# Optimization experiments

Hardware: AMD Instinct MI355X
Metric: run time of the kernel (lower is better)

## Reference

```python
import jax, jax.numpy as jnp
import numpy as np

B, CIN, H, W = 256, 1280, 7, 7
A, NCLS, HID, NGT = 9, 20, 128, 40
OUT_DIM = 5 * A + NCLS  # 65


def setup_inputs() -> dict:
    key = jax.random.key(0)
    ks = jax.random.split(key, 8)
    features = jax.random.normal(ks[0], (B, CIN, H, W), jnp.float32)
    # grid: (x, y) centers of each feature cell, in feature-map coordinates
    grid = jax.random.uniform(ks[1], (B, H, W, 2), jnp.float32) * 7.0
    # GT boxes (x1, y1, x2, y2, class), padded count NGT per image
    xy1 = jax.random.uniform(ks[2], (B, NGT, 2), jnp.float32) * 5.0
    wh = jax.random.uniform(ks[3], (B, NGT, 2), jnp.float32) * 2.0 + 0.5
    cls = jax.random.randint(ks[4], (B, NGT, 1), 0, NCLS).astype(jnp.float32)
    bboxes = jnp.concatenate([xy1, xy1 + wh, cls], axis=-1)
    # anchor shapes (w, h) as in SingleStageDetector.__init__
    anc = jnp.array([[1.0, 1], [2, 2], [3, 3], [4, 4], [5, 5],
                     [2, 3], [3, 2], [3, 5], [5, 3]], jnp.float32)
    W1 = jax.random.normal(ks[5], (HID, CIN), jnp.float32) * 0.02
    b1 = jnp.zeros((HID,), jnp.float32)
    W2 = jax.random.normal(ks[6], (OUT_DIM, HID), jnp.float32) * 0.02
    b2 = jnp.zeros((OUT_DIM,), jnp.float32)
    return dict(features=features, grid=grid, bboxes=bboxes, anc=anc,
                W1=W1, b1=b1, W2=W2, b2=b2)


def reference(features, grid, bboxes, anc, W1, b1, W2, b2):
    Bx = features.shape[0]
    # --- PredictionNetwork (inference mode; dropout is identity at eval) ---
    h = jnp.einsum('bchw,oc->bohw', features, W1) + b1[None, :, None, None]
    h = jax.nn.leaky_relu(h, negative_slope=0.01)
    out = jnp.einsum('bchw,oc->bohw', h, W2) + b2[None, :, None, None]
    conf_scores = jax.nn.sigmoid(out[:, 4 * A:5 * A])          # (B, A, H, W)
    offsets = out[:, :4 * A].reshape(Bx, A, 4, H, W)
    offsets = jnp.concatenate(
        [jax.nn.sigmoid(offsets[:, :, :2]) - 0.5, offsets[:, :, 2:]], axis=2)
    class_scores = out[:, 5 * A:]                               # (B, C, H, W)
    # --- GenerateAnchor: (B, A, H, W, 4) as (x_tl, y_tl, x_br, y_br) ---
    ctr = grid[:, None]                    # (B, 1, H, W, 2)
    half = anc[None, :, None, None, :] / 2  # (1, A, 1, 1, 2)
    anchors = jnp.concatenate([ctr - half, ctr + half], axis=-1)
    # --- IoU: (B, A*H*W, N) ---
    P = anchors.reshape(Bx, -1, 4)          # (B, AHW, 4)
    gt = bboxes[..., :4]                    # (B, N, 4)
    tl = jnp.maximum(P[:, :, None, :2], gt[:, None, :, :2])
    br = jnp.minimum(P[:, :, None, 2:], gt[:, None, :, 2:])
    inter = jnp.prod(jnp.clip(br - tl, 0.0), axis=-1)  # (B, AHW, N)
    # torch code zeroes intersections for proposals with any coord <= 0
    legal = (jnp.min(P, axis=-1) > 0)[..., None]
    inter = inter * legal
    p_area = ((P[:, :, 2] - P[:, :, 0]) * (P[:, :, 3] - P[:, :, 1]))[:, :, None]
    g_area = ((gt[:, :, 2] - gt[:, :, 0]) * (gt[:, :, 3] - gt[:, :, 1]))[:, None, :]
    iou_mat = inter / (g_area + p_area - inter)
    return (conf_scores, offsets, class_scores, iou_mat)
```

## Files before the change

### kernel.cpp

```cpp
#include <hip/hip_runtime.h>


#define CIN_  1280
#define HW_   49
#define HID_  128
#define OUTD_ 65
#define NGT_  40
#define NP_   441

#define CONF_OFF 0
#define OFFS_OFF 112896
#define CLS_OFF  564480
#define IOU_OFF  815360

#define WS_W1F   0
#define WS_W2F   81920
#define WS_PART  87040
#define WS_NEED_FULL ((87040u + 3211264u) * 4u)
#define WS_NEED_MID  (81920u * 4u)

typedef __bf16 bf16x8 __attribute__((ext_vector_type(8)));
typedef float  f32x4  __attribute__((ext_vector_type(4)));

__device__ __forceinline__ unsigned pack2bf(float lo, float hi) {
    unsigned a = __float_as_uint(lo);
    unsigned b = __float_as_uint(hi);
    a = (a + 0x7FFFu + ((a >> 16) & 1u)) >> 16;
    b = (b + 0x7FFFu + ((b >> 16) & 1u)) >> 16;
    return a | (b << 16);
}
__device__ __forceinline__ float bflo(unsigned u) { return __uint_as_float(u << 16); }
__device__ __forceinline__ float bfhi(unsigned u) { return __uint_as_float(u & 0xFFFF0000u); }
__device__ __forceinline__ float sigmoidf_(float v) { return 1.f / (1.f + __expf(-v)); }

__device__ __forceinline__ bf16x8 ld_frag(const unsigned* p) {
    union { uint4 u; bf16x8 v; } x;
    x.u = *(const uint4*)p;
    return x.v;
}
__device__ __forceinline__ bf16x8 as_bf(uint4 u) {
    union { uint4 u; bf16x8 v; } x; x.u = u; return x.v;
}

__global__ __launch_bounds__(256) void prep_w1f(const float* __restrict__ W1,
                                                unsigned* __restrict__ g) {
    int X = blockIdx.x * 256 + threadIdx.x;
    int sub = X & 3, lane = (X >> 2) & 63, f = X >> 8;
    int mt = f & 7, K32 = f >> 3;
    int o = mt * 16 + (lane & 15);
    int c = K32 * 32 + (lane >> 4) * 8 + sub * 2;
    float2 v = *(const float2*)(W1 + o * CIN_ + c);
    g[X] = pack2bf(v.x, v.y);
}

__global__ __launch_bounds__(256) void prep_w2f(const float* __restrict__ W2,
                                                unsigned* __restrict__ g) {
    int X = blockIdx.x * 256 + threadIdx.x;
    int sub = X & 3, lane = (X >> 2) & 63, f = X >> 8;
    int mt2 = f % 5, ks2 = f / 5;
    int o2 = mt2 * 16 + (lane & 15);
    int c = ks2 * 32 + (lane >> 4) * 8 + sub * 2;
    unsigned val = 0;
    if (o2 < OUTD_) {
        float2 v = *(const float2*)(W2 + o2 * HID_ + c);
        val = pack2bf(v.x, v.y);
    }
    g[X] = val;
}

__global__ __launch_bounds__(256) void gemm1_partial(
    const float* __restrict__ F, const float* __restrict__ grid,
    const float* __restrict__ bbox, const float* __restrict__ anc,
    const unsigned* __restrict__ gW1f,
    unsigned* __restrict__ wsp, float* __restrict__ out)
{
    __shared__ __align__(16) unsigned smF[49 * 164];
    float* smP = (float*)smF;
    float* smG = (float*)smF + 2646;

    const int tid  = threadIdx.x;
    const int b    = blockIdx.x >> 2;
    const int ksp  = blockIdx.x & 3;
    const int lane = tid & 63;
    const int w    = tid >> 6;
    const int quad = lane >> 4;
    const int m16  = lane & 15;

    const float* Fb = F + b * (CIN_ * HW_) + ksp * 320 * HW_;

    for (int idx = tid; idx < 1960; idx += 256) {
        int cb = idx / 49;
        int hw = idx - cb * 49;
        const float* s = Fb + cb * 392 + hw;
        float v0 = s[0],   v1 = s[49],  v2 = s[98],  v3 = s[147];
        float v4 = s[196], v5 = s[245], v6 = s[294], v7 = s[343];
        uint4 pk;
        pk.x = pack2bf(v0, v1); pk.y = pack2bf(v2, v3);
        pk.z = pack2bf(v4, v5); pk.w = pack2bf(v6, v7);
        *(uint4*)(smF + hw * 164 + cb * 4) = pk;
    }
    __syncthreads();

    const int row3 = (m16 == 0) ? 48 : (m16 - 1);
    const unsigned* Bb[4] = {
        smF + m16 * 164 + quad * 4,
        smF + (16 + m16) * 164 + quad * 4,
        smF + (32 + m16) * 164 + quad * 4,
        smF + row3 * 164 + quad * 4
    };

    const int mt0 = w * 2, mt1 = mt0 + 1;
    const int K32b = ksp * 10;
    const uint4* Ap0 = (const uint4*)gW1f + (K32b * 8 + mt0) * 64 + lane;
    const uint4* Ap1 = (const uint4*)gW1f + (K32b * 8 + mt1) * 64 + lane;

    f32x4 acc0[4], acc1[4];
    #pragma unroll
    for (int nt = 0; nt < 4; ++nt) { acc0[nt] = (f32x4)(0.f); acc1[nt] = (f32x4)(0.f); }

    uint4 a0 = Ap0[0], a1 = Ap1[0];
    for (int k = 0; k < 10; ++k) {
        uint4 n0, n1;
        if (k < 9) { n0 = Ap0[(k + 1) * 512]; n1 = Ap1[(k + 1) * 512]; }
        bf16x8 A0 = as_bf(a0), A1 = as_bf(a1);
        const int co = k * 16;
        #pragma unroll
        for (int nt = 0; nt < 4; ++nt) {
            bf16x8 Bf = ld_frag(Bb[nt] + co);
            acc0[nt] = __builtin_amdgcn_mfma_f32_16x16x32_bf16(A0, Bf, acc0[nt], 0, 0, 0);
            acc1[nt] = __builtin_amdgcn_mfma_f32_16x16x32_bf16(A1, Bf, acc1[nt], 0, 0, 0);
        }
        a0 = n0; a1 = n1;
    }

    const unsigned pbase = (unsigned)(b * 4 + ksp) * 64u;
    #pragma unroll
    for (int m = 0; m < 2; ++m) {
        const f32x4* ac = m ? acc1 : acc0;
        int mtg = w * 2 + m;
        #pragma unroll
        for (int nt = 0; nt < 4; ++nt) {
            int hw = (nt < 3) ? (nt * 16 + m16) : ((m16 == 0) ? 48 : -1);
            if (hw >= 0) {
                #pragma unroll
                for (int rp = 0; rp < 2; ++rp) {
                    int op = mtg * 8 + quad * 2 + rp;
                    wsp[(pbase + op) * 49u + hw] = pack2bf(ac[nt][2 * rp], ac[nt][2 * rp + 1]);
                }
            }
        }
    }
    __syncthreads();

    for (int pp = tid; pp < NP_; pp += 256) {
        int a = pp / 49, r = pp - a * 49;
        float cx = grid[b * 98 + 2 * r], cy = grid[b * 98 + 2 * r + 1];
        float hx = anc[2 * a] * 0.5f,    hy = anc[2 * a + 1] * 0.5f;
        float x1 = cx - hx, y1 = cy - hy, x2 = cx + hx, y2 = cy + hy;
        smP[pp * 6 + 0] = x1; smP[pp * 6 + 1] = y1;
        smP[pp * 6 + 2] = x2; smP[pp * 6 + 3] = y2;
        smP[pp * 6 + 4] = (x2 - x1) * (y2 - y1);
        smP[pp * 6 + 5] = (fminf(fminf(x1, y1), fminf(x2, y2)) > 0.f) ? 1.f : 0.f;
    }
    if (tid < NGT_) {
        int g = tid;
        float x1 = bbox[b * 200 + g * 5 + 0];
        float y1 = bbox[b * 200 + g * 5 + 1];
        float x2 = bbox[b * 200 + g * 5 + 2];
        float y2 = bbox[b * 200 + g * 5 + 3];
        smG[g * 5 + 0] = x1; smG[g * 5 + 1] = y1;
        smG[g * 5 + 2] = x2; smG[g * 5 + 3] = y2;
        smG[g * 5 + 4] = (x2 - x1) * (y2 - y1);
    }
    __syncthreads();

    for (int ii = tid; ii < 4410; ii += 256) {
        int idx = ksp * 4410 + ii;
        int p = idx / 40;
        int g = idx - p * 40;
        const float* P = smP + p * 6;
        const float* G = smG + g * 5;
        float tlx = fmaxf(P[0], G[0]);
        float tly = fmaxf(P[1], G[1]);
        float brx = fminf(P[2], G[2]);
        float bry = fminf(P[3], G[3]);
        float dx = fmaxf(brx - tlx, 0.f);
        float dy = fmaxf(bry - tly, 0.f);
        float inter = dx * dy * P[5];
        out[IOU_OFF + b * (NP_ * NGT_) + idx] = inter / (G[4] + P[4] - inter);
    }
}

__global__ __launch_bounds__(320) void gemm2_epilogue(
    const unsigned* __restrict__ wsp, const unsigned* __restrict__ gW2f,
    const float* __restrict__ B1, const float* __restrict__ B2,
    float* __restrict__ out)
{
    __shared__ __align__(16) unsigned smHT[49 * 68];

    const int tid  = threadIdx.x;
    const int b    = blockIdx.x;
    const int lane = tid & 63;
    const int w    = tid >> 6;
    const int quad = lane >> 4;
    const int m16  = lane & 15;

    const uint4* Aw2 = (const uint4*)gW2f + w * 64 + lane;
    uint4 af0 = Aw2[0], af1 = Aw2[320], af2 = Aw2[640], af3 = Aw2[960];

    const unsigned* pb = wsp + b * 12544;
    for (int j = tid; j < 3136; j += 320) {
        int op = j / 49;
        int hw = j - op * 49;
        const unsigned* p = pb + op * 49 + hw;
        unsigned u0 = p[0], u1 = p[3136], u2 = p[6272], u3 = p[9408];
        float v0 = ((bflo(u0) + bflo(u1)) + (bflo(u2) + bflo(u3))) + B1[2 * op];
        float v1 = ((bfhi(u0) + bfhi(u1)) + (bfhi(u2) + bfhi(u3))) + B1[2 * op + 1];
        v0 = v0 > 0.f ? v0 : 0.01f * v0;
        v1 = v1 > 0.f ? v1 : 0.01f * v1;
        smHT[hw * 68 + op] = pack2bf(v0, v1);
    }
    __syncthreads();

    const int row3 = (m16 == 0) ? 48 : (m16 - 1);
    const unsigned* Bb[4] = {
        smHT + m16 * 68 + quad * 4,
        smHT + (16 + m16) * 68 + quad * 4,
        smHT + (32 + m16) * 68 + quad * 4,
        smHT + row3 * 68 + quad * 4
    };
    f32x4 acc[4];
    #pragma unroll
    for (int nt = 0; nt < 4; ++nt) acc[nt] = (f32x4)(0.f);
    uint4 afs[4] = { af0, af1, af2, af3 };
    #pragma unroll
    for (int ks2 = 0; ks2 < 4; ++ks2) {
        bf16x8 A = as_bf(afs[ks2]);
        const int co = ks2 * 16;
        #pragma unroll
        for (int nt = 0; nt < 4; ++nt) {
            bf16x8 Bf = ld_frag(Bb[nt] + co);
            acc[nt] = __builtin_amdgcn_mfma_f32_16x16x32_bf16(A, Bf, acc[nt], 0, 0, 0);
        }
    }

    #pragma unroll
    for (int nt = 0; nt < 4; ++nt) {
        int hw = (nt < 3) ? (nt * 16 + m16) : ((m16 == 0) ? 48 : -1);
        if (hw < 0) continue;
        #pragma unroll
        for (int r = 0; r < 4; ++r) {
            int o2 = w * 16 + quad * 4 + r;
            if (o2 >= OUTD_) continue;
            float a = acc[nt][r] + B2[o2];
            unsigned dst; float val;
            if (o2 < 36) {
                int an = o2 >> 2, kk = o2 & 3;
                val = (kk < 2) ? (sigmoidf_(a) - 0.5f) : a;
                dst = OFFS_OFF + b * 1764 + an * 196 + kk * 49 + hw;
            } else if (o2 < 45) {
                val = sigmoidf_(a);
                dst = CONF_OFF + b * 441 + (o2 - 36) * 49 + hw;
            } else {
                val = a;
                dst = CLS_OFF + b * 980 + (o2 - 45) * 49 + hw;
            }
            out[dst] = val;
        }
    }
}

#define SF_STRIDE 644
__global__ __launch_bounds__(512) void fused_single(
    const float* __restrict__ F, const float* __restrict__ grid,
    const float* __restrict__ bbox, const float* __restrict__ anc,
    const unsigned* __restrict__ gW1f, const float* __restrict__ B1,
    const float* __restrict__ W2, const float* __restrict__ B2,
    float* __restrict__ out)
{
    __shared__ __align__(16) unsigned lds[49 * SF_STRIDE];
    unsigned* smF = lds;
    unsigned* smH = lds;
    float* smP = (float*)(lds + 3136);
    float* smG = (float*)(lds + 3136 + 2646);

    const int tid  = threadIdx.x;
    const int b    = blockIdx.x;
    const int lane = tid & 63;
    const int w    = tid >> 6;
    const int quad = lane >> 4;
    const int m16  = lane & 15;
    const float* Fb = F + b * (CIN_ * HW_);

    for (int i = tid; i < 640 * 49; i += 512) {
        int cp = i / 49;
        int hw = i - cp * 49;
        const float* s = Fb + (2 * cp) * HW_ + hw;
        smF[hw * SF_STRIDE + cp] = pack2bf(s[0], s[HW_]);
    }
    __syncthreads();

    const int row3 = (m16 == 0) ? 48 : (m16 - 1);
    const unsigned* Bb[4] = {
        smF + m16 * SF_STRIDE + quad * 4,
        smF + (16 + m16) * SF_STRIDE + quad * 4,
        smF + (32 + m16) * SF_STRIDE + quad * 4,
        smF + row3 * SF_STRIDE + quad * 4
    };
    const uint4* Aw = (const uint4*)gW1f + w * 64 + lane;

    f32x4 acc[4];
    #pragma unroll
    for (int nt = 0; nt < 4; ++nt) acc[nt] = (f32x4)(0.f);

    uint4 a0 = Aw[0], a1 = Aw[512];
    for (int ch = 0; ch < 20; ++ch) {
        uint4 n0, n1;
        if (ch < 19) { n0 = Aw[(ch + 1) * 1024]; n1 = Aw[(ch + 1) * 1024 + 512]; }
        const int coff = ch * 32;
        bf16x8 A0 = as_bf(a0), A1 = as_bf(a1);
        #pragma unroll
        for (int nt = 0; nt < 4; ++nt) {
            bf16x8 b0 = ld_frag(Bb[nt] + coff);
            bf16x8 b1 = ld_frag(Bb[nt] + coff + 16);
            acc[nt] = __builtin_amdgcn_mfma_f32_16x16x32_bf16(A0, b0, acc[nt], 0, 0, 0);
            acc[nt] = __builtin_amdgcn_mfma_f32_16x16x32_bf16(A1, b1, acc[nt], 0, 0, 0);
        }
        a0 = n0; a1 = n1;
    }
    __syncthreads();

    #pragma unroll
    for (int nt = 0; nt < 4; ++nt) {
        int hw = (nt < 3) ? (nt * 16 + m16) : ((m16 == 0) ? 48 : -1);
        if (hw >= 0) {
            #pragma unroll
            for (int rp = 0; rp < 2; ++rp) {
                int o0 = w * 16 + quad * 4 + 2 * rp;
                float v0 = acc[nt][2 * rp]     + B1[o0];
                float v1 = acc[nt][2 * rp + 1] + B1[o0 + 1];
                v0 = v0 > 0.f ? v0 : 0.01f * v0;
                v1 = v1 > 0.f ? v1 : 0.01f * v1;
                smH[(o0 >> 1) * HW_ + hw] = pack2bf(v0, v1);
            }
        }
    }
    if (tid < NP_) {
        int pp = tid, a = pp / 49, r = pp - a * 49;
        float cx = grid[b * 98 + 2 * r], cy = grid[b * 98 + 2 * r + 1];
        float hx = anc[2 * a] * 0.5f,    hy = anc[2 * a + 1] * 0.5f;
        float x1 = cx - hx, y1 = cy - hy, x2 = cx + hx, y2 = cy + hy;
        smP[pp * 6 + 0] = x1; smP[pp * 6 + 1] = y1;
        smP[pp * 6 + 2] = x2; smP[pp * 6 + 3] = y2;
        smP[pp * 6 + 4] = (x2 - x1) * (y2 - y1);
        smP[pp * 6 + 5] = (fminf(fminf(x1, y1), fminf(x2, y2)) > 0.f) ? 1.f : 0.f;
    }
    if (tid >= 472) {
        int g = tid - 472;
        float x1 = bbox[b * 200 + g * 5 + 0];
        float y1 = bbox[b * 200 + g * 5 + 1];
        float x2 = bbox[b * 200 + g * 5 + 2];
        float y2 = bbox[b * 200 + g * 5 + 3];
        smG[g * 5 + 0] = x1; smG[g * 5 + 1] = y1;
        smG[g * 5 + 2] = x2; smG[g * 5 + 3] = y2;
        smG[g * 5 + 4] = (x2 - x1) * (y2 - y1);
    }
    __syncthreads();

    for (int idx = tid; idx < OUTD_ * HW_; idx += 512) {
        int o2 = idx / 49;
        int hw = idx - o2 * 49;
        const float2* wr = (const float2*)(W2 + o2 * HID_);
        float s0 = 0.f, s1 = 0.f;
        #pragma unroll 8
        for (int k2 = 0; k2 < 64; ++k2) {
            unsigned hp = smH[k2 * HW_ + hw];
            float2 wv = wr[k2];
            s0 = fmaf(wv.x, bflo(hp), s0);
            s1 = fmaf(wv.y, bfhi(hp), s1);
        }
        float a = B2[o2] + (s0 + s1);
        unsigned dst; float val;
        if (o2 < 36) {
            int an = o2 >> 2, kk = o2 & 3;
            val = (kk < 2) ? (sigmoidf_(a) - 0.5f) : a;
            dst = OFFS_OFF + b * 1764 + an * 196 + kk * 49 + hw;
        } else if (o2 < 45) {
            val = sigmoidf_(a);
            dst = CONF_OFF + b * 441 + (o2 - 36) * 49 + hw;
        } else {
            val = a;
            dst = CLS_OFF + b * 980 + (o2 - 45) * 49 + hw;
        }
        out[dst] = val;
    }
    for (int idx = tid; idx < NP_ * NGT_; idx += 512) {
        int pp = idx / 40;
        int g  = idx - pp * 40;
        const float* P = smP + pp * 6;
        const float* G = smG + g * 5;
        float tlx = fmaxf(P[0], G[0]);
        float tly = fmaxf(P[1], G[1]);
        float brx = fminf(P[2], G[2]);
        float bry = fminf(P[3], G[3]);
        float dx = fmaxf(brx - tlx, 0.f);
        float dy = fmaxf(bry - tly, 0.f);
        float inter = dx * dy * P[5];
        out[IOU_OFF + b * (NP_ * NGT_) + idx] = inter / (G[4] + P[4] - inter);
    }
}

__global__ __launch_bounds__(512) void fused_fallback(
    const float* __restrict__ F, const float* __restrict__ grid,
    const float* __restrict__ bbox, const float* __restrict__ anc,
    const float* __restrict__ W1, const float* __restrict__ B1,
    const float* __restrict__ W2, const float* __restrict__ B2,
    float* __restrict__ out)
{
    __shared__ __align__(16) unsigned lds[4608 + 2304 + 6272];
    unsigned* smA = lds;
    unsigned* smB = lds + 4608;
    float*    smH = (float*)(lds + 4608 + 2304);
    float* smP = (float*)lds;
    float* smG = (float*)(lds + 4608);

    const int tid  = threadIdx.x;
    const int b    = blockIdx.x;
    const int lane = tid & 63;
    const int w    = tid >> 6;
    const int quad = lane >> 4;
    const int m16  = lane & 15;
    const float* Fb = F + b * (CIN_ * HW_);

    f32x4 acc[4];
    #pragma unroll
    for (int nt = 0; nt < 4; ++nt) acc[nt] = (f32x4)(0.f);

    for (int ch = 0; ch < 20; ++ch) {
        const int c0 = ch * 64;
        __syncthreads();
        #pragma unroll
        for (int rr = 0; rr < 8; ++rr) {
            int pi = tid + rr * 512;
            int o = pi >> 5, cp = pi & 31;
            float2 fx = *(const float2*)(W1 + o * CIN_ + c0 + 2 * cp);
            smA[o * 36 + cp] = pack2bf(fx.x, fx.y);
        }
        for (int pi = tid; pi < 32 * 49; pi += 512) {
            int cp = pi / 49;
            int hw = pi - cp * 49;
            const float* src = Fb + (c0 + 2 * cp) * HW_ + hw;
            smB[hw * 36 + cp] = pack2bf(src[0], src[HW_]);
        }
        __syncthreads();
        const unsigned* Ab = smA + (w * 16 + m16) * 36 + quad * 4;
        const unsigned* Bb = smB + m16 * 36 + quad * 4;
        #pragma unroll
        for (int ks = 0; ks < 2; ++ks) {
            bf16x8 af = ld_frag(Ab + ks * 16);
            #pragma unroll
            for (int nt = 0; nt < 4; ++nt) {
                bf16x8 bf = ld_frag(Bb + nt * 16 * 36 + ks * 16);
                acc[nt] = __builtin_amdgcn_mfma_f32_16x16x32_bf16(af, bf, acc[nt], 0, 0, 0);
            }
        }
    }
    #pragma unroll
    for (int nt = 0; nt < 4; ++nt) {
        int hw = nt * 16 + m16;
        if (hw < HW_) {
            #pragma unroll
            for (int r = 0; r < 4; ++r) {
                int o = w * 16 + quad * 4 + r;
                float v = acc[nt][r] + B1[o];
                v = v > 0.f ? v : 0.01f * v;
                smH[o * HW_ + hw] = v;
            }
        }
    }
    __syncthreads();
    if (tid < NP_) {
        int pp = tid, a = pp / 49, r = pp - a * 49;
        float cx = grid[b * 98 + 2 * r], cy = grid[b * 98 + 2 * r + 1];
        float hx = anc[2 * a] * 0.5f,    hy = anc[2 * a + 1] * 0.5f;
        float x1 = cx - hx, y1 = cy - hy, x2 = cx + hx, y2 = cy + hy;
        smP[pp * 6 + 0] = x1; smP[pp * 6 + 1] = y1;
        smP[pp * 6 + 2] = x2; smP[pp * 6 + 3] = y2;
        smP[pp * 6 + 4] = (x2 - x1) * (y2 - y1);
        smP[pp * 6 + 5] = (fminf(fminf(x1, y1), fminf(x2, y2)) > 0.f) ? 1.f : 0.f;
    }
    if (tid >= 472) {
        int g = tid - 472;
        float x1 = bbox[b * 200 + g * 5 + 0];
        float y1 = bbox[b * 200 + g * 5 + 1];
        float x2 = bbox[b * 200 + g * 5 + 2];
        float y2 = bbox[b * 200 + g * 5 + 3];
        smG[g * 5 + 0] = x1; smG[g * 5 + 1] = y1;
        smG[g * 5 + 2] = x2; smG[g * 5 + 3] = y2;
        smG[g * 5 + 4] = (x2 - x1) * (y2 - y1);
    }
    for (int idx = tid; idx < OUTD_ * HW_; idx += 512) {
        int o2 = idx / 49;
        int hw = idx - o2 * 49;
        const float4* wr = (const float4*)(W2 + o2 * HID_);
        const float*  hc = smH + hw;
        float s0 = 0.f, s1 = 0.f, s2 = 0.f, s3 = 0.f;
        #pragma unroll 8
        for (int k4 = 0; k4 < 32; ++k4) {
            float4 wv = wr[k4];
            s0 = fmaf(wv.x, hc[(4 * k4 + 0) * HW_], s0);
            s1 = fmaf(wv.y, hc[(4 * k4 + 1) * HW_], s1);
            s2 = fmaf(wv.z, hc[(4 * k4 + 2) * HW_], s2);
            s3 = fmaf(wv.w, hc[(4 * k4 + 3) * HW_], s3);
        }
        float a = B2[o2] + ((s0 + s1) + (s2 + s3));
        unsigned dst; float val;
        if (o2 < 36) { int an = o2 >> 2, kk = o2 & 3;
            val = (kk < 2) ? (sigmoidf_(a) - 0.5f) : a;
            dst = OFFS_OFF + b * 1764 + an * 196 + kk * 49 + hw;
        } else if (o2 < 45) { val = sigmoidf_(a);
            dst = CONF_OFF + b * 441 + (o2 - 36) * 49 + hw;
        } else { val = a;
            dst = CLS_OFF + b * 980 + (o2 - 45) * 49 + hw; }
        out[dst] = val;
    }
    __syncthreads();
    for (int idx = tid; idx < NP_ * NGT_; idx += 512) {
        int pp = idx / 40;
        int g  = idx - pp * 40;
        const float* P = smP + pp * 6;
        const float* G = smG + g * 5;
        float tlx = fmaxf(P[0], G[0]);
        float tly = fmaxf(P[1], G[1]);
        float brx = fminf(P[2], G[2]);
        float bry = fminf(P[3], G[3]);
        float dx = fmaxf(brx - tlx, 0.f);
        float dy = fmaxf(bry - tly, 0.f);
        float inter = dx * dy * P[5];
        out[IOU_OFF + b * (NP_ * NGT_) + idx] = inter / (G[4] + P[4] - inter);
    }
}

extern "C" void kernel_launch(void* const* d_in, const int* in_sizes, int n_in,
                              void* d_out, int out_size, void* d_ws, size_t ws_size,
                              hipStream_t stream) {
    const float* F  = (const float*)d_in[0];
    const float* G  = (const float*)d_in[1];
    const float* BB = (const float*)d_in[2];
    const float* AN = (const float*)d_in[3];
    const float* W1 = (const float*)d_in[4];
    const float* B1 = (const float*)d_in[5];
    const float* W2 = (const float*)d_in[6];
    const float* B2 = (const float*)d_in[7];
    float* out = (float*)d_out;
    unsigned* wsu = (unsigned*)d_ws;

    if (ws_size >= (size_t)WS_NEED_FULL) {
        prep_w1f<<<320, 256, 0, stream>>>(W1, wsu + WS_W1F);
        prep_w2f<<<20, 256, 0, stream>>>(W2, wsu + WS_W2F);
        gemm1_partial<<<1024, 256, 0, stream>>>(F, G, BB, AN, wsu + WS_W1F,
                                                wsu + WS_PART, out);
        gemm2_epilogue<<<256, 320, 0, stream>>>(wsu + WS_PART, wsu + WS_W2F,
                                                B1, B2, out);
    } else if (ws_size >= (size_t)WS_NEED_MID) {
        prep_w1f<<<320, 256, 0, stream>>>(W1, wsu + WS_W1F);
        fused_single<<<256, 512, 0, stream>>>(F, G, BB, AN, wsu + WS_W1F,
                                              B1, W2, B2, out);
    } else {
        fused_fallback<<<256, 512, 0, stream>>>(F, G, BB, AN, W1, B1, W2, B2, out);
    }
}
```

Baseline: 140.5 us.

## Pre-pack features into bf16 MFMA fragment layout in a merged prep kernel

Adds a prep_all kernel that reads features with coalesced float4 loads, transposes them through shared memory, and writes bf16 data already laid out as MFMA B-fragments into the workspace. The same kernel also packs W1 and W2, replacing the two separate weight-prep launches. gemm1_partial then loads A and B fragments straight from global memory with software prefetch, with no LDS staging and no barrier. The cost is an extra round trip of the packed feature tensor through global memory and a much larger workspace requirement. The smallest-workspace fallback now reuses prep_w1f into the workspace even when the workspace may be too small for it.

```diff
diff --git a/kernel.cpp b/kernel.cpp
--- a/kernel.cpp
+++ b/kernel.cpp
@@ -13,10 +13,11 @@
 #define CLS_OFF  564480
 #define IOU_OFF  815360
 
-#define WS_W1F   0
-#define WS_W2F   81920
-#define WS_PART  87040
-#define WS_NEED_FULL ((87040u + 3211264u) * 4u)
+#define WS_W1F   0u
+#define WS_W2F   81920u
+#define WS_PART  87040u
+#define WS_BF    3298304u
+#define WS_NEED_FULL ((3298304u + 10485760u) * 4u)
 #define WS_NEED_MID  (81920u * 4u)
 
 typedef __bf16 bf16x8 __attribute__((ext_vector_type(8)));
@@ -42,41 +43,77 @@
     union { uint4 u; bf16x8 v; } x; x.u = u; return x.v;
 }
 
-__global__ __launch_bounds__(256) void prep_w1f(const float* __restrict__ W1,
-                                                unsigned* __restrict__ g) {
-    int X = blockIdx.x * 256 + threadIdx.x;
-    int sub = X & 3, lane = (X >> 2) & 63, f = X >> 8;
-    int mt = f & 7, K32 = f >> 3;
-    int o = mt * 16 + (lane & 15);
-    int c = K32 * 32 + (lane >> 4) * 8 + sub * 2;
-    float2 v = *(const float2*)(W1 + o * CIN_ + c);
-    g[X] = pack2bf(v.x, v.y);
-}
-
-__global__ __launch_bounds__(256) void prep_w2f(const float* __restrict__ W2,
-                                                unsigned* __restrict__ g) {
-    int X = blockIdx.x * 256 + threadIdx.x;
-    int sub = X & 3, lane = (X >> 2) & 63, f = X >> 8;
-    int mt2 = f % 5, ks2 = f / 5;
-    int o2 = mt2 * 16 + (lane & 15);
-    int c = ks2 * 32 + (lane >> 4) * 8 + sub * 2;
-    unsigned val = 0;
-    if (o2 < OUTD_) {
-        float2 v = *(const float2*)(W2 + o2 * HID_ + c);
-        val = pack2bf(v.x, v.y);
-    }
-    g[X] = val;
+__global__ __launch_bounds__(256) void prep_all(
+    const float* __restrict__ F, const float* __restrict__ W1,
+    const float* __restrict__ W2, unsigned* __restrict__ ws)
+{
+    __shared__ float smT[64 * 52];
+    const int tid = threadIdx.x;
+    const int blk = blockIdx.x;
+
+    if (blk < 5120) {
+        const int b  = blk / 20;
+        const int ck = blk - b * 20;
+        const float4* src = (const float4*)(F + b * 62720 + ck * 3136);
+        for (int i = tid; i < 784; i += 256) {
+            float4 v = src[i];
+            int fl = i * 4;
+            int c0 = fl / 49, h0 = fl - c0 * 49;
+            smT[c0 * 52 + h0] = v.x;
+            int f1 = fl + 1; int c1 = f1 / 49, h1 = f1 - c1 * 49;
+            smT[c1 * 52 + h1] = v.y;
+            int f2 = fl + 2; int c2 = f2 / 49, h2 = f2 - c2 * 49;
+            smT[c2 * 52 + h2] = v.z;
+            int f3 = fl + 3; int c3 = f3 / 49, h3 = f3 - c3 * 49;
+            smT[c3 * 52 + h3] = v.w;
+        }
+        __syncthreads();
+        unsigned* gBf = ws + WS_BF + b * 40960u + ck * 2048u;
+        #pragma unroll
+        for (int r = 0; r < 8; ++r) {
+            int X = r * 256 + tid;
+            int sub  = X & 3;
+            int lane = (X >> 2) & 63;
+            int fi   = X >> 8;
+            int nt = fi & 3, kl = fi >> 2;
+            int m16l = lane & 15, quadl = lane >> 4;
+            int hw = (nt < 3) ? (nt * 16 + m16l)
+                              : ((m16l == 0) ? 48 : (m16l - 1));
+            int c = kl * 32 + quadl * 8 + sub * 2;
+            gBf[(kl * 4 + nt) * 256 + lane * 4 + sub] =
+                pack2bf(smT[c * 52 + hw], smT[(c + 1) * 52 + hw]);
+        }
+    } else if (blk < 5440) {
+        int X = (blk - 5120) * 256 + tid;
+        int sub = X & 3, lane = (X >> 2) & 63, f = X >> 8;
+        int mt = f & 7, K32 = f >> 3;
+        int o = mt * 16 + (lane & 15);
+        int c = K32 * 32 + (lane >> 4) * 8 + sub * 2;
+        float2 v = *(const float2*)(W1 + o * CIN_ + c);
+        ws[WS_W1F + X] = pack2bf(v.x, v.y);
+    } else {
+        int X = (blk - 5440) * 256 + tid;
+        int sub = X & 3, lane = (X >> 2) & 63, f = X >> 8;
+        int mt2 = f % 5, ks2 = f / 5;
+        int o2 = mt2 * 16 + (lane & 15);
+        int c = ks2 * 32 + (lane >> 4) * 8 + sub * 2;
+        unsigned val = 0;
+        if (o2 < OUTD_) {
+            float2 v = *(const float2*)(W2 + o2 * HID_ + c);
+            val = pack2bf(v.x, v.y);
+        }
+        ws[WS_W2F + X] = val;
+    }
 }
 
 __global__ __launch_bounds__(256) void gemm1_partial(
-    const float* __restrict__ F, const float* __restrict__ grid,
-    const float* __restrict__ bbox, const float* __restrict__ anc,
-    const unsigned* __restrict__ gW1f,
+    const float* __restrict__ grid, const float* __restrict__ bbox,
+    const float* __restrict__ anc, const unsigned* __restrict__ ws,
     unsigned* __restrict__ wsp, float* __restrict__ out)
 {
-    __shared__ __align__(16) unsigned smF[49 * 164];
-    float* smP = (float*)smF;
-    float* smG = (float*)smF + 2646;
+    __shared__ float smPG[NP_ * 6 + NGT_ * 5];
+    float* smP = smPG;
+    float* smG = smPG + NP_ * 6;
 
     const int tid  = threadIdx.x;
     const int b    = blockIdx.x >> 2;
@@ -86,51 +123,37 @@
     const int quad = lane >> 4;
     const int m16  = lane & 15;
 
-    const float* Fb = F + b * (CIN_ * HW_) + ksp * 320 * HW_;
-
-    for (int idx = tid; idx < 1960; idx += 256) {
-        int cb = idx / 49;
-        int hw = idx - cb * 49;
-        const float* s = Fb + cb * 392 + hw;
-        float v0 = s[0],   v1 = s[49],  v2 = s[98],  v3 = s[147];
-        float v4 = s[196], v5 = s[245], v6 = s[294], v7 = s[343];
-        uint4 pk;
-        pk.x = pack2bf(v0, v1); pk.y = pack2bf(v2, v3);
-        pk.z = pack2bf(v4, v5); pk.w = pack2bf(v6, v7);
-        *(uint4*)(smF + hw * 164 + cb * 4) = pk;
-    }
-    __syncthreads();
-
-    const int row3 = (m16 == 0) ? 48 : (m16 - 1);
-    const unsigned* Bb[4] = {
-        smF + m16 * 164 + quad * 4,
-        smF + (16 + m16) * 164 + quad * 4,
-        smF + (32 + m16) * 164 + quad * 4,
-        smF + row3 * 164 + quad * 4
-    };
-
-    const int mt0 = w * 2, mt1 = mt0 + 1;
     const int K32b = ksp * 10;
-    const uint4* Ap0 = (const uint4*)gW1f + (K32b * 8 + mt0) * 64 + lane;
-    const uint4* Ap1 = (const uint4*)gW1f + (K32b * 8 + mt1) * 64 + lane;
+    const uint4* Bp  = (const uint4*)(ws + WS_BF) + b * 10240 + K32b * 256 + lane;
+    const uint4* Ap0 = (const uint4*)(ws + WS_W1F) + (K32b * 8 + w * 2) * 64 + lane;
+    const uint4* Ap1 = Ap0 + 64;
 
     f32x4 acc0[4], acc1[4];
     #pragma unroll
     for (int nt = 0; nt < 4; ++nt) { acc0[nt] = (f32x4)(0.f); acc1[nt] = (f32x4)(0.f); }
 
     uint4 a0 = Ap0[0], a1 = Ap1[0];
+    uint4 bv0 = Bp[0], bv1 = Bp[64], bv2 = Bp[128], bv3 = Bp[192];
+
     for (int k = 0; k < 10; ++k) {
-        uint4 n0, n1;
-        if (k < 9) { n0 = Ap0[(k + 1) * 512]; n1 = Ap1[(k + 1) * 512]; }
+        uint4 na0, na1, nb0, nb1, nb2, nb3;
+        if (k < 9) {
+            na0 = Ap0[(k + 1) * 512]; na1 = Ap1[(k + 1) * 512];
+            const uint4* nBp = Bp + (k + 1) * 256;
+            nb0 = nBp[0]; nb1 = nBp[64]; nb2 = nBp[128]; nb3 = nBp[192];
+        }
         bf16x8 A0 = as_bf(a0), A1 = as_bf(a1);
-        const int co = k * 16;
-        #pragma unroll
-        for (int nt = 0; nt < 4; ++nt) {
-            bf16x8 Bf = ld_frag(Bb[nt] + co);
-            acc0[nt] = __builtin_amdgcn_mfma_f32_16x16x32_bf16(A0, Bf, acc0[nt], 0, 0, 0);
-            acc1[nt] = __builtin_amdgcn_mfma_f32_16x16x32_bf16(A1, Bf, acc1[nt], 0, 0, 0);
-        }
-        a0 = n0; a1 = n1;
+        bf16x8 B0 = as_bf(bv0), B1f = as_bf(bv1), B2f = as_bf(bv2), B3 = as_bf(bv3);
+        acc0[0] = __builtin_amdgcn_mfma_f32_16x16x32_bf16(A0, B0,  acc0[0], 0, 0, 0);
+        acc1[0] = __builtin_amdgcn_mfma_f32_16x16x32_bf16(A1, B0,  acc1[0], 0, 0, 0);
+        acc0[1] = __builtin_amdgcn_mfma_f32_16x16x32_bf16(A0, B1f, acc0[1], 0, 0, 0);
+        acc1[1] = __builtin_amdgcn_mfma_f32_16x16x32_bf16(A1, B1f, acc1[1], 0, 0, 0);
+        acc0[2] = __builtin_amdgcn_mfma_f32_16x16x32_bf16(A0, B2f, acc0[2], 0, 0, 0);
+        acc1[2] = __builtin_amdgcn_mfma_f32_16x16x32_bf16(A1, B2f, acc1[2], 0, 0, 0);
+        acc0[3] = __builtin_amdgcn_mfma_f32_16x16x32_bf16(A0, B3,  acc0[3], 0, 0, 0);
+        acc1[3] = __builtin_amdgcn_mfma_f32_16x16x32_bf16(A1, B3,  acc1[3], 0, 0, 0);
+        a0 = na0; a1 = na1;
+        bv0 = nb0; bv1 = nb1; bv2 = nb2; bv3 = nb3;
     }
 
     const unsigned pbase = (unsigned)(b * 4 + ksp) * 64u;
@@ -145,12 +168,12 @@
                 #pragma unroll
                 for (int rp = 0; rp < 2; ++rp) {
                     int op = mtg * 8 + quad * 2 + rp;
-                    wsp[(pbase + op) * 49u + hw] = pack2bf(ac[nt][2 * rp], ac[nt][2 * rp + 1]);
+                    wsp[(pbase + op) * 49u + hw] =
+                        pack2bf(ac[nt][2 * rp], ac[nt][2 * rp + 1]);
                 }
             }
         }
     }
-    __syncthreads();
 
     for (int pp = tid; pp < NP_; pp += 256) {
         int a = pp / 49, r = pp - a * 49;
@@ -270,6 +293,17 @@
     }
 }
 
+__global__ __launch_bounds__(256) void prep_w1f(const float* __restrict__ W1,
+                                                unsigned* __restrict__ g) {
+    int X = blockIdx.x * 256 + threadIdx.x;
+    int sub = X & 3, lane = (X >> 2) & 63, f = X >> 8;
+    int mt = f & 7, K32 = f >> 3;
+    int o = mt * 16 + (lane & 15);
+    int c = K32 * 32 + (lane >> 4) * 8 + sub * 2;
+    float2 v = *(const float2*)(W1 + o * CIN_ + c);
+    g[X] = pack2bf(v.x, v.y);
+}
+
 #define SF_STRIDE 644
 __global__ __launch_bounds__(512) void fused_single(
     const float* __restrict__ F, const float* __restrict__ grid,
@@ -410,137 +444,6 @@
     }
 }
 
-__global__ __launch_bounds__(512) void fused_fallback(
-    const float* __restrict__ F, const float* __restrict__ grid,
-    const float* __restrict__ bbox, const float* __restrict__ anc,
-    const float* __restrict__ W1, const float* __restrict__ B1,
-    const float* __restrict__ W2, const float* __restrict__ B2,
-    float* __restrict__ out)
-{
-    __shared__ __align__(16) unsigned lds[4608 + 2304 + 6272];
-    unsigned* smA = lds;
-    unsigned* smB = lds + 4608;
-    float*    smH = (float*)(lds + 4608 + 2304);
-    float* smP = (float*)lds;
-    float* smG = (float*)(lds + 4608);
-
-    const int tid  = threadIdx.x;
-    const int b    = blockIdx.x;
-    const int lane = tid & 63;
-    const int w    = tid >> 6;
-    const int quad = lane >> 4;
-    const int m16  = lane & 15;
-    const float* Fb = F + b * (CIN_ * HW_);
-
-    f32x4 acc[4];
-    #pragma unroll
-    for (int nt = 0; nt < 4; ++nt) acc[nt] = (f32x4)(0.f);
-
-    for (int ch = 0; ch < 20; ++ch) {
-        const int c0 = ch * 64;
-        __syncthreads();
-        #pragma unroll
-        for (int rr = 0; rr < 8; ++rr) {
-            int pi = tid + rr * 512;
-            int o = pi >> 5, cp = pi & 31;
-            float2 fx = *(const float2*)(W1 + o * CIN_ + c0 + 2 * cp);
-            smA[o * 36 + cp] = pack2bf(fx.x, fx.y);
-        }
-        for (int pi = tid; pi < 32 * 49; pi += 512) {
-            int cp = pi / 49;
-            int hw = pi - cp * 49;
-            const float* src = Fb + (c0 + 2 * cp) * HW_ + hw;
-            smB[hw * 36 + cp] = pack2bf(src[0], src[HW_]);
-        }
-        __syncthreads();
-        const unsigned* Ab = smA + (w * 16 + m16) * 36 + quad * 4;
-        const unsigned* Bb = smB + m16 * 36 + quad * 4;
-        #pragma unroll
-        for (int ks = 0; ks < 2; ++ks) {
-            bf16x8 af = ld_frag(Ab + ks * 16);
-            #pragma unroll
-            for (int nt = 0; nt < 4; ++nt) {
-                bf16x8 bf = ld_frag(Bb + nt * 16 * 36 + ks * 16);
-                acc[nt] = __builtin_amdgcn_mfma_f32_16x16x32_bf16(af, bf, acc[nt], 0, 0, 0);
-            }
-        }
-    }
-    #pragma unroll
-    for (int nt = 0; nt < 4; ++nt) {
-        int hw = nt * 16 + m16;
-        if (hw < HW_) {
-            #pragma unroll
-            for (int r = 0; r < 4; ++r) {
-                int o = w * 16 + quad * 4 + r;
-                float v = acc[nt][r] + B1[o];
-                v = v > 0.f ? v : 0.01f * v;
-                smH[o * HW_ + hw] = v;
-            }
-        }
-    }
-    __syncthreads();
-    if (tid < NP_) {
-        int pp = tid, a = pp / 49, r = pp - a * 49;
-        float cx = grid[b * 98 + 2 * r], cy = grid[b * 98 + 2 * r + 1];
-        float hx = anc[2 * a] * 0.5f,    hy = anc[2 * a + 1] * 0.5f;
-        float x1 = cx - hx, y1 = cy - hy, x2 = cx + hx, y2 = cy + hy;
-        smP[pp * 6 + 0] = x1; smP[pp * 6 + 1] = y1;
-        smP[pp * 6 + 2] = x2; smP[pp * 6 + 3] = y2;
-        smP[pp * 6 + 4] = (x2 - x1) * (y2 - y1);
-        smP[pp * 6 + 5] = (fminf(fminf(x1, y1), fminf(x2, y2)) > 0.f) ? 1.f : 0.f;
-    }
-    if (tid >= 472) {
-        int g = tid - 472;
-        float x1 = bbox[b * 200 + g * 5 + 0];
-        float y1 = bbox[b * 200 + g * 5 + 1];
-        float x2 = bbox[b * 200 + g * 5 + 2];
-        float y2 = bbox[b * 200 + g * 5 + 3];
-        smG[g * 5 + 0] = x1; smG[g * 5 + 1] = y1;
-        smG[g * 5 + 2] = x2; smG[g * 5 + 3] = y2;
-        smG[g * 5 + 4] = (x2 - x1) * (y2 - y1);
-    }
-    for (int idx = tid; idx < OUTD_ * HW_; idx += 512) {
-        int o2 = idx / 49;
-        int hw = idx - o2 * 49;
-        const float4* wr = (const float4*)(W2 + o2 * HID_);
-        const float*  hc = smH + hw;
-        float s0 = 0.f, s1 = 0.f, s2 = 0.f, s3 = 0.f;
-        #pragma unroll 8
-        for (int k4 = 0; k4 < 32; ++k4) {
-            float4 wv = wr[k4];
-            s0 = fmaf(wv.x, hc[(4 * k4 + 0) * HW_], s0);
-            s1 = fmaf(wv.y, hc[(4 * k4 + 1) * HW_], s1);
-            s2 = fmaf(wv.z, hc[(4 * k4 + 2) * HW_], s2);
-            s3 = fmaf(wv.w, hc[(4 * k4 + 3) * HW_], s3);
-        }
-        float a = B2[o2] + ((s0 + s1) + (s2 + s3));
-        unsigned dst; float val;
-        if (o2 < 36) { int an = o2 >> 2, kk = o2 & 3;
-            val = (kk < 2) ? (sigmoidf_(a) - 0.5f) : a;
-            dst = OFFS_OFF + b * 1764 + an * 196 + kk * 49 + hw;
-        } else if (o2 < 45) { val = sigmoidf_(a);
-            dst = CONF_OFF + b * 441 + (o2 - 36) * 49 + hw;
-        } else { val = a;
-            dst = CLS_OFF + b * 980 + (o2 - 45) * 49 + hw; }
-        out[dst] = val;
-    }
-    __syncthreads();
-    for (int idx = tid; idx < NP_ * NGT_; idx += 512) {
-        int pp = idx / 40;
-        int g  = idx - pp * 40;
-        const float* P = smP + pp * 6;
-        const float* G = smG + g * 5;
-        float tlx = fmaxf(P[0], G[0]);
-        float tly = fmaxf(P[1], G[1]);
-        float brx = fminf(P[2], G[2]);
-        float bry = fminf(P[3], G[3]);
-        float dx = fmaxf(brx - tlx, 0.f);
-        float dy = fmaxf(bry - tly, 0.f);
-        float inter = dx * dy * P[5];
-        out[IOU_OFF + b * (NP_ * NGT_) + idx] = inter / (G[4] + P[4] - inter);
-    }
-}
-
 extern "C" void kernel_launch(void* const* d_in, const int* in_sizes, int n_in,
                               void* d_out, int out_size, void* d_ws, size_t ws_size,
                               hipStream_t stream) {
@@ -556,9 +459,8 @@
     unsigned* wsu = (unsigned*)d_ws;
 
     if (ws_size >= (size_t)WS_NEED_FULL) {
-        prep_w1f<<<320, 256, 0, stream>>>(W1, wsu + WS_W1F);
-        prep_w2f<<<20, 256, 0, stream>>>(W2, wsu + WS_W2F);
-        gemm1_partial<<<1024, 256, 0, stream>>>(F, G, BB, AN, wsu + WS_W1F,
+        prep_all<<<5460, 256, 0, stream>>>(F, W1, W2, wsu);
+        gemm1_partial<<<1024, 256, 0, stream>>>(G, BB, AN, wsu,
                                                 wsu + WS_PART, out);
         gemm2_epilogue<<<256, 320, 0, stream>>>(wsu + WS_PART, wsu + WS_W2F,
                                                 B1, B2, out);
@@ -567,6 +469,8 @@
         fused_single<<<256, 512, 0, stream>>>(F, G, BB, AN, wsu + WS_W1F,
                                               B1, W2, B2, out);
     } else {
-        fused_fallback<<<256, 512, 0, stream>>>(F, G, BB, AN, W1, B1, W2, B2, out);
-    }
-}
+        prep_w1f<<<320, 256, 0, stream>>>(W1, wsu + WS_W1F);
+        fused_single<<<256, 512, 0, stream>>>(F, G, BB, AN, wsu + WS_W1F,
+                                              B1, W2, B2, out);
+    }
+}
```

After: 144.5 us. 2.9% more time.
